# Performance work log

Measured on AMD Instinct MI355X. Metric: run time of the kernel, lower is better.

The kernel has to match this reference:

```python
import jax, jax.numpy as jnp
import numpy as np

N_NODES = 50000
N_EDGES = 800000
N_RELS = 200
D = 128


def setup_inputs() -> dict:
    key = jax.random.key(0)
    ks = jax.random.split(key, 9)
    h = jax.random.normal(ks[0], (N_NODES, D), dtype=jnp.float32)
    r = jax.random.normal(ks[1], (N_RELS, D), dtype=jnp.float32)
    norm = jax.random.uniform(ks[2], (N_NODES, 1), dtype=jnp.float32)
    src = jax.random.randint(ks[3], (N_EDGES,), 0, N_NODES, dtype=jnp.int32)
    dst = jax.random.randint(ks[4], (N_EDGES,), 0, N_NODES, dtype=jnp.int32)
    rel = jax.random.randint(ks[5], (N_EDGES,), 0, N_RELS, dtype=jnp.int32)
    stdv = 1.0 / np.sqrt(D)
    W_msg = jax.random.uniform(ks[6], (D, D), minval=-stdv, maxval=stdv, dtype=jnp.float32)
    W = jax.random.uniform(ks[7], (D, D), minval=-stdv, maxval=stdv, dtype=jnp.float32)
    b = jax.random.uniform(ks[8], (D,), minval=-stdv, maxval=stdv, dtype=jnp.float32)
    return {"h": h, "r": r, "norm": norm, "src": src, "dst": dst, "rel": rel,
            "W_msg": W_msg, "W": W, "b": b}


def reference(h, r, norm, src, dst, rel, W_msg, W, b):
    # dropout=0.0 (eval); h = h * norm (symmetric-norm pre-scale)
    hn = h * norm                                    # [N, D]
    # per-edge message: (h_src - r_rel) @ W_msg
    msg = (hn[src] - r[rel]) @ W_msg                 # [E, D]
    # scatter-sum to destination nodes, then post-scale by norm
    agg = jax.ops.segment_sum(msg, dst, num_segments=hn.shape[0]) * norm  # [N, D]
    out = hn @ W + agg + b
    return jax.nn.relu(out)
```

## Files before the change

kernel.cpp:

```cpp
#include <hip/hip_runtime.h>

#define N_NODES 50000
#define N_EDGES 800000
#define DIM 128
#define K2 256
#define NREL 200
#define NB2 391
#define EPB 2048
#define BN4 16
#define NB4 3128
#define ECAP4 512

typedef unsigned short u16;
typedef __attribute__((ext_vector_type(8))) short short8;
typedef __attribute__((ext_vector_type(4))) float f32x4;

__device__ __forceinline__ float bf2f(u16 v) {
    union { unsigned int u; float f; } x;
    x.u = ((unsigned int)v) << 16;
    return x.f;
}

__device__ __forceinline__ u16 f2bf(float f) {
    union { unsigned int u; float f; } x;
    x.f = f;
    return (u16)((x.u + 0x7FFFu + ((x.u >> 16) & 1u)) >> 16);
}

__device__ __forceinline__ int sniff_fp32(const void* h, int tid) {
    const u16* hp = (const u16*)h;
    u16 v = hp[2 * (tid & 63)];
    float a = fabsf(bf2f(v));
    int insane = ((v & 0x7F80) == 0x7F80) || (a != 0.0f && (a > 1e6f || a < 1e-20f));
    return __popcll(__ballot(insane)) > 16;
}

#define PREP_H (N_NODES * 32)
#define PREP_R (NREL * 32)
#define PREP_W 8192
#define PREP_N (N_NODES / 4)
#define PREP_B 32
#define PREP_TOT (PREP_H + PREP_R + PREP_W + PREP_N + PREP_B)
#define PREP_BLOCKS ((PREP_TOT + 255) / 256)
#define HIST_BLOCKS 128
__global__ __launch_bounds__(256) void prep_hist(
    const void* __restrict__ h, const void* __restrict__ r, const void* __restrict__ norm,
    const void* __restrict__ W, const void* __restrict__ Wmsg, const void* __restrict__ bias,
    const int* __restrict__ dst,
    u16* __restrict__ hx, u16* __restrict__ r_bf, u16* __restrict__ wt,
    u16* __restrict__ norm_bf, float* __restrict__ b_f, int* __restrict__ bucketCount)
{
    __shared__ int hh[NB2];
    int tid = threadIdx.x;
    if (blockIdx.x >= PREP_BLOCKS) {
        for (int i = tid; i < NB2; i += 256) hh[i] = 0;
        __syncthreads();
        int stride = HIST_BLOCKS * 256;
        for (int e = (blockIdx.x - PREP_BLOCKS) * 256 + tid; e < N_EDGES; e += stride)
            atomicAdd(&hh[dst[e] >> 7], 1);
        __syncthreads();
        for (int i = tid; i < NB2; i += 256)
            if (hh[i]) atomicAdd(&bucketCount[i], hh[i]);
        return;
    }
    int isf = sniff_fp32(h, tid);
    int t = blockIdx.x * 256 + tid;
    if (t < PREP_H) {
        int n = t >> 5, c = t & 31;
        float4 v; float nv;
        if (isf) {
            nv = ((const float*)norm)[n];
            v = *(const float4*)((const float*)h + (size_t)n * DIM + c * 4);
        } else {
            nv = bf2f(((const u16*)norm)[n]);
            ushort4 u = *(const ushort4*)((const u16*)h + (size_t)n * DIM + c * 4);
            v = make_float4(bf2f(u.x), bf2f(u.y), bf2f(u.z), bf2f(u.w));
        }
        ushort4 o;
        o.x = f2bf(v.x * nv); o.y = f2bf(v.y * nv); o.z = f2bf(v.z * nv); o.w = f2bf(v.w * nv);
        *(ushort4*)(hx + (size_t)n * DIM + c * 4) = o;
    } else if (t < PREP_H + PREP_R) {
        int t2 = t - PREP_H;
        int rho = t2 >> 5, c = t2 & 31;
        float4 v;
        if (isf) v = *(const float4*)((const float*)r + (size_t)rho * DIM + c * 4);
        else {
            ushort4 u = *(const ushort4*)((const u16*)r + (size_t)rho * DIM + c * 4);
            v = make_float4(bf2f(u.x), bf2f(u.y), bf2f(u.z), bf2f(u.w));
        }
        ushort4 o;
        o.x = f2bf(v.x); o.y = f2bf(v.y); o.z = f2bf(v.z); o.w = f2bf(v.w);
        *(ushort4*)(r_bf + (size_t)rho * DIM + c * 4) = o;
    } else if (t < PREP_H + PREP_R + PREP_W) {
        int t3 = t - PREP_H - PREP_R;
        int j = t3 >> 6;
        int k0 = (t3 & 63) * 4;
        ushort4 o;
        u16* op = (u16*)&o;
        for (int kk = 0; kk < 4; ++kk) {
            int k = k0 + kk;
            float wv;
            if (isf) wv = (k < 128) ? ((const float*)W)[(size_t)k * DIM + j]
                                    : ((const float*)Wmsg)[(size_t)(k - 128) * DIM + j];
            else     wv = (k < 128) ? bf2f(((const u16*)W)[(size_t)k * DIM + j])
                                    : bf2f(((const u16*)Wmsg)[(size_t)(k - 128) * DIM + j]);
            op[kk] = f2bf(wv);
        }
        *(ushort4*)(wt + (size_t)j * K2 + k0) = o;
    } else if (t < PREP_H + PREP_R + PREP_W + PREP_N) {
        int n0 = (t - PREP_H - PREP_R - PREP_W) * 4;
        ushort4 o;
        if (isf) {
            float4 v = *(const float4*)((const float*)norm + n0);
            o.x = f2bf(v.x); o.y = f2bf(v.y); o.z = f2bf(v.z); o.w = f2bf(v.w);
        } else {
            o = *(const ushort4*)((const u16*)norm + n0);
        }
        *(ushort4*)(norm_bf + n0) = o;
    } else if (t < PREP_TOT) {
        int j0 = (t - PREP_H - PREP_R - PREP_W - PREP_N) * 4;
        float4 v;
        if (isf) v = *(const float4*)((const float*)bias + j0);
        else {
            ushort4 u = *(const ushort4*)((const u16*)bias + j0);
            v = make_float4(bf2f(u.x), bf2f(u.y), bf2f(u.z), bf2f(u.w));
        }
        *(float4*)(b_f + j0) = v;
    }
}

__global__ __launch_bounds__(512) void bucket_scan(const int* __restrict__ bucketCount,
                            int* __restrict__ bucketBase, int* __restrict__ bucketCursor) {
    __shared__ int sd[512];
    int t = threadIdx.x;
    int c = (t < NB2) ? bucketCount[t] : 0;
    sd[t] = c;
    __syncthreads();
    for (int off = 1; off < 512; off <<= 1) {
        int v = (t >= off) ? sd[t - off] : 0;
        __syncthreads();
        sd[t] += v;
        __syncthreads();
    }
    if (t < NB2) { int ex = sd[t] - c; bucketBase[t] = ex; bucketCursor[t] = ex; }
    if (t == 0) bucketBase[NB2] = N_EDGES;
}

__global__ __launch_bounds__(512) void fill_lds(
    const int* __restrict__ dst, const int* __restrict__ src, const int* __restrict__ rel,
    int* __restrict__ bucketCursor, int* __restrict__ spk)
{
    __shared__ int hist[NB2];
    __shared__ int lbase[NB2];
    __shared__ int gbase[NB2];
    __shared__ int sd[512];
    __shared__ int pay[EPB];
    __shared__ u16 bkt[EPB];
    int tid = threadIdx.x;
    for (int i = tid; i < NB2; i += 512) hist[i] = 0;
    __syncthreads();
    int e0 = blockIdx.x * EPB;
    int myb[4], myr[4], myp[4];
#pragma unroll
    for (int i = 0; i < 4; ++i) {
        int e = e0 + i * 512 + tid;
        myb[i] = -1;
        if (e < N_EDGES) {
            int d = dst[e];
            int b = d >> 7;
            myb[i] = b;
            myr[i] = atomicAdd(&hist[b], 1);
            myp[i] = src[e] | (rel[e] << 16) | ((d & 127) << 24);
        }
    }
    __syncthreads();
    sd[tid] = (tid < NB2) ? hist[tid] : 0;
    __syncthreads();
    for (int off = 1; off < 512; off <<= 1) {
        int v = (tid >= off) ? sd[tid - off] : 0;
        __syncthreads();
        sd[tid] += v;
        __syncthreads();
    }
    if (tid < NB2) {
        lbase[tid] = sd[tid] - hist[tid];
        gbase[tid] = hist[tid] ? atomicAdd(&bucketCursor[tid], hist[tid]) : 0;
    }
    __syncthreads();
#pragma unroll
    for (int i = 0; i < 4; ++i) {
        if (myb[i] >= 0) {
            int lp = lbase[myb[i]] + myr[i];
            pay[lp] = myp[i];
            bkt[lp] = (u16)myb[i];
        }
    }
    __syncthreads();
    int total = N_EDGES - e0; if (total > EPB) total = EPB;
#pragma unroll
    for (int i = 0; i < 4; ++i) {
        int lp = i * 512 + tid;
        if (lp < total) {
            int b = bkt[lp];
            spk[gbase[b] + (lp - lbase[b])] = pay[lp];
        }
    }
}

__global__ __launch_bounds__(256) void bucket_fused(
    const u16* __restrict__ hx, const u16* __restrict__ r_bf,
    const u16* __restrict__ norm_bf, const float* __restrict__ b_f,
    const int* __restrict__ bucketBase, const int* __restrict__ spk,
    const u16* __restrict__ wt, const void* __restrict__ h, void* __restrict__ out)
{
    __shared__ int sorted[ECAP4];
    __shared__ int hist[BN4];
    __shared__ int nbase[BN4];
    __shared__ u16 Xu[BN4][136];
    int tid = threadIdx.x;
    int b = blockIdx.x;
    int fb = b >> 3, oct = b & 7;
    int base = bucketBase[fb], end = bucketBase[fb + 1];
    int size = end - base;

    if (tid < BN4) hist[tid] = 0;
    __syncthreads();
    for (int i = tid; i < size; i += 256) {
        int dl = (spk[base + i] >> 24) & 127;
        if ((dl >> 4) == oct) atomicAdd(&hist[dl & 15], 1);
    }
    __syncthreads();
    if (tid < BN4) nbase[tid] = hist[tid];
    __syncthreads();
    for (int off = 1; off < BN4; off <<= 1) {
        int v = 0;
        if (tid < BN4 && tid >= off) v = nbase[tid - off];
        __syncthreads();
        if (tid < BN4) nbase[tid] += v;
        __syncthreads();
    }
    if (tid < BN4) { nbase[tid] -= hist[tid]; hist[tid] = 0; }
    __syncthreads();
    for (int i = tid; i < size; i += 256) {
        int pk = spk[base + i];
        int dl = (pk >> 24) & 127;
        if ((dl >> 4) == oct) {
            int d4 = dl & 15;
            int rk = atomicAdd(&hist[d4], 1);
            int pos = nbase[d4] + rk;
            if (pos < ECAP4) sorted[pos] = pk;
        }
    }
    __syncthreads();

    int g = tid & 15, grp = tid >> 4;
    {
        int d4 = grp;
        int rs = nbase[d4], cnt = hist[d4];
        float acc[8] = {};
        int j = 0;
        for (; j + 3 < cnt; j += 4) {
            int pk0 = sorted[rs + j], pk1 = sorted[rs + j + 1];
            int pk2 = sorted[rs + j + 2], pk3 = sorted[rs + j + 3];
            short8 h0 = *(const short8*)(hx + (size_t)(pk0 & 0xFFFF) * DIM + g * 8);
            short8 h1 = *(const short8*)(hx + (size_t)(pk1 & 0xFFFF) * DIM + g * 8);
            short8 h2 = *(const short8*)(hx + (size_t)(pk2 & 0xFFFF) * DIM + g * 8);
            short8 h3 = *(const short8*)(hx + (size_t)(pk3 & 0xFFFF) * DIM + g * 8);
            short8 v0 = *(const short8*)(r_bf + (size_t)((pk0 >> 16) & 0xFF) * DIM + g * 8);
            short8 v1 = *(const short8*)(r_bf + (size_t)((pk1 >> 16) & 0xFF) * DIM + g * 8);
            short8 v2 = *(const short8*)(r_bf + (size_t)((pk2 >> 16) & 0xFF) * DIM + g * 8);
            short8 v3 = *(const short8*)(r_bf + (size_t)((pk3 >> 16) & 0xFF) * DIM + g * 8);
#pragma unroll
            for (int d = 0; d < 8; ++d) {
                acc[d] += (bf2f((u16)h0[d]) - bf2f((u16)v0[d]))
                        + (bf2f((u16)h1[d]) - bf2f((u16)v1[d]))
                        + (bf2f((u16)h2[d]) - bf2f((u16)v2[d]))
                        + (bf2f((u16)h3[d]) - bf2f((u16)v3[d]));
            }
        }
        for (; j < cnt; ++j) {
            int pk = sorted[rs + j];
            short8 hv = *(const short8*)(hx + (size_t)(pk & 0xFFFF) * DIM + g * 8);
            short8 rv = *(const short8*)(r_bf + (size_t)((pk >> 16) & 0xFF) * DIM + g * 8);
#pragma unroll
            for (int d = 0; d < 8; ++d) acc[d] += bf2f((u16)hv[d]) - bf2f((u16)rv[d]);
        }
        int node = b * BN4 + d4;
        float nv = bf2f(norm_bf[node < N_NODES ? node : 0]);
        short8 o;
#pragma unroll
        for (int d = 0; d < 8; ++d) o[d] = (short)f2bf(acc[d] * nv);
        *(short8*)&Xu[d4][g * 8] = o;
    }
    __syncthreads();

    int w = tid >> 6, lane = tid & 63;
    int m = lane & 15, quad = lane >> 4;
    int nodeA = b * BN4 + m;
    short8 a[8];
#pragma unroll
    for (int kb = 0; kb < 4; ++kb)
        a[kb] = *(const short8*)(hx + (size_t)nodeA * DIM + kb * 32 + quad * 8);
#pragma unroll
    for (int kb = 0; kb < 4; ++kb)
        a[4 + kb] = *(const short8*)&Xu[m][kb * 32 + quad * 8];
    int isf = sniff_fp32(h, tid);
#pragma unroll
    for (int ct = 0; ct < 2; ++ct) {
        int n0 = w * 32 + ct * 16;
        f32x4 c4 = {0.f, 0.f, 0.f, 0.f};
#pragma unroll
        for (int kb = 0; kb < 8; ++kb) {
            short8 bv = *(const short8*)(wt + (size_t)(n0 + m) * K2 + kb * 32 + quad * 8);
            c4 = __builtin_amdgcn_mfma_f32_16x16x32_bf16(a[kb], bv, c4, 0, 0, 0);
        }
        int col = n0 + m;
        float bb = b_f[col];
#pragma unroll
        for (int rg = 0; rg < 4; ++rg) {
            int n = b * BN4 + quad * 4 + rg;
            if (n < N_NODES) {
                float v = c4[rg] + bb;
                v = v > 0.f ? v : 0.f;
                if (isf) ((float*)out)[(size_t)n * DIM + col] = v;
                else     ((u16*)out)[(size_t)n * DIM + col] = f2bf(v);
            }
        }
    }
}

static inline size_t alup(size_t x) { return (x + 255) & ~(size_t)255; }

extern "C" void kernel_launch(void* const* d_in, const int* in_sizes, int n_in,
                              void* d_out, int out_size, void* d_ws, size_t ws_size,
                              hipStream_t stream) {
    const void* h    = d_in[0];
    const void* r    = d_in[1];
    const void* norm = d_in[2];
    const int* src   = (const int*)d_in[3];
    const int* dst   = (const int*)d_in[4];
    const int* rel   = (const int*)d_in[5];
    const void* Wmsg = d_in[6];
    const void* W    = d_in[7];
    const void* b    = d_in[8];

    char* p = (char*)d_ws;
    u16* hx       = (u16*)p;                 p += alup((size_t)N_NODES * DIM * 2);
    u16* r_bf     = (u16*)p;                 p += alup((size_t)NREL * DIM * 2);
    u16* wt       = (u16*)p;                 p += alup((size_t)DIM * K2 * 2);
    u16* norm_bf  = (u16*)p;                 p += alup((size_t)N_NODES * 2);
    float* b_f    = (float*)p;               p += alup((size_t)DIM * 4);
    int* bucketCount  = (int*)p;             p += alup((size_t)NB2 * 4);
    int* bucketBase   = (int*)p;             p += alup((size_t)(NB2 + 1) * 4);
    int* bucketCursor = (int*)p;             p += alup((size_t)NB2 * 4);
    int* spk      = (int*)p;                 p += alup((size_t)N_EDGES * 4);

    hipMemsetAsync(bucketCount, 0, (size_t)NB2 * 4, stream);
    prep_hist<<<PREP_BLOCKS + HIST_BLOCKS, 256, 0, stream>>>(
        h, r, norm, W, Wmsg, b, dst, hx, r_bf, wt, norm_bf, b_f, bucketCount);
    bucket_scan<<<1, 512, 0, stream>>>(bucketCount, bucketBase, bucketCursor);
    fill_lds<<<(N_EDGES + EPB - 1) / EPB, 512, 0, stream>>>(dst, src, rel, bucketCursor, spk);
    bucket_fused<<<NB4, 256, 0, stream>>>(
        hx, r_bf, norm_bf, b_f, bucketBase, spk, wt, h, d_out);
}
```

Baseline: 194.5 us.

## Bucket edges by 16-node groups and accumulate with LDS float atomics

Edges are now bucketed directly by 16-node destination groups (3125 buckets) instead of 128-node buckets followed by a per-block re-sort. The separate scan kernel is merged into the fill kernel: every block redundantly scans the bucket counts and scatters edges through global atomics on per-bucket cursors, so the LDS local sort is gone. In the fused kernel, edges are accumulated into an fp32 LDS tile with shared-memory atomics rather than via per-node sorted lists. This removes one launch and the in-block counting sort, at the cost of many more global atomics, redundant scans in each block, and LDS atomic contention.

```diff
diff --git a/kernel.cpp b/kernel.cpp
--- a/kernel.cpp
+++ b/kernel.cpp
@@ -5,11 +5,10 @@
 #define DIM 128
 #define K2 256
 #define NREL 200
-#define NB2 391
-#define EPB 2048
-#define BN4 16
-#define NB4 3128
-#define ECAP4 512
+#define NBF 3125
+#define BN 16
+#define FEB 2048
+#define FILL_BLOCKS ((N_EDGES + FEB - 1) / FEB)
 
 typedef unsigned short u16;
 typedef __attribute__((ext_vector_type(8))) short short8;
@@ -50,16 +49,16 @@
     u16* __restrict__ hx, u16* __restrict__ r_bf, u16* __restrict__ wt,
     u16* __restrict__ norm_bf, float* __restrict__ b_f, int* __restrict__ bucketCount)
 {
-    __shared__ int hh[NB2];
+    __shared__ int hh[NBF];
     int tid = threadIdx.x;
     if (blockIdx.x >= PREP_BLOCKS) {
-        for (int i = tid; i < NB2; i += 256) hh[i] = 0;
+        for (int i = tid; i < NBF; i += 256) hh[i] = 0;
         __syncthreads();
         int stride = HIST_BLOCKS * 256;
         for (int e = (blockIdx.x - PREP_BLOCKS) * 256 + tid; e < N_EDGES; e += stride)
-            atomicAdd(&hh[dst[e] >> 7], 1);
+            atomicAdd(&hh[dst[e] >> 4], 1);
         __syncthreads();
-        for (int i = tid; i < NB2; i += 256)
+        for (int i = tid; i < NBF; i += 256)
             if (hh[i]) atomicAdd(&bucketCount[i], hh[i]);
         return;
     }
@@ -129,52 +128,22 @@
     }
 }
 
-__global__ __launch_bounds__(512) void bucket_scan(const int* __restrict__ bucketCount,
-                            int* __restrict__ bucketBase, int* __restrict__ bucketCursor) {
-    __shared__ int sd[512];
-    int t = threadIdx.x;
-    int c = (t < NB2) ? bucketCount[t] : 0;
-    sd[t] = c;
-    __syncthreads();
-    for (int off = 1; off < 512; off <<= 1) {
-        int v = (t >= off) ? sd[t - off] : 0;
-        __syncthreads();
-        sd[t] += v;
-        __syncthreads();
-    }
-    if (t < NB2) { int ex = sd[t] - c; bucketBase[t] = ex; bucketCursor[t] = ex; }
-    if (t == 0) bucketBase[NB2] = N_EDGES;
-}
-
-__global__ __launch_bounds__(512) void fill_lds(
+__global__ __launch_bounds__(512) void fill_scatter(
     const int* __restrict__ dst, const int* __restrict__ src, const int* __restrict__ rel,
+    const int* __restrict__ bucketCount, int* __restrict__ bucketBase,
     int* __restrict__ bucketCursor, int* __restrict__ spk)
 {
-    __shared__ int hist[NB2];
-    __shared__ int lbase[NB2];
-    __shared__ int gbase[NB2];
+    __shared__ int sbase[NBF];
     __shared__ int sd[512];
-    __shared__ int pay[EPB];
-    __shared__ u16 bkt[EPB];
     int tid = threadIdx.x;
-    for (int i = tid; i < NB2; i += 512) hist[i] = 0;
-    __syncthreads();
-    int e0 = blockIdx.x * EPB;
-    int myb[4], myr[4], myp[4];
-#pragma unroll
-    for (int i = 0; i < 4; ++i) {
-        int e = e0 + i * 512 + tid;
-        myb[i] = -1;
-        if (e < N_EDGES) {
-            int d = dst[e];
-            int b = d >> 7;
-            myb[i] = b;
-            myr[i] = atomicAdd(&hist[b], 1);
-            myp[i] = src[e] | (rel[e] << 16) | ((d & 127) << 24);
-        }
-    }
-    __syncthreads();
-    sd[tid] = (tid < NB2) ? hist[tid] : 0;
+    int lv[7]; int ls = 0;
+#pragma unroll
+    for (int i = 0; i < 7; ++i) {
+        int idx = tid * 7 + i;
+        lv[i] = (idx < NBF) ? bucketCount[idx] : 0;
+        ls += lv[i];
+    }
+    sd[tid] = ls;
     __syncthreads();
     for (int off = 1; off < 512; off <<= 1) {
         int v = (tid >= off) ? sd[tid - off] : 0;
@@ -182,27 +151,27 @@
         sd[tid] += v;
         __syncthreads();
     }
-    if (tid < NB2) {
-        lbase[tid] = sd[tid] - hist[tid];
-        gbase[tid] = hist[tid] ? atomicAdd(&bucketCursor[tid], hist[tid]) : 0;
+    int ex = sd[tid] - ls;
+#pragma unroll
+    for (int i = 0; i < 7; ++i) {
+        int idx = tid * 7 + i;
+        if (idx < NBF) sbase[idx] = ex;
+        ex += lv[i];
     }
     __syncthreads();
+    if (blockIdx.x == 0) {
+        for (int i = tid; i < NBF; i += 512) bucketBase[i] = sbase[i];
+        if (tid == 0) bucketBase[NBF] = N_EDGES;
+    }
+    int e0 = blockIdx.x * FEB;
 #pragma unroll
     for (int i = 0; i < 4; ++i) {
-        if (myb[i] >= 0) {
-            int lp = lbase[myb[i]] + myr[i];
-            pay[lp] = myp[i];
-            bkt[lp] = (u16)myb[i];
-        }
-    }
-    __syncthreads();
-    int total = N_EDGES - e0; if (total > EPB) total = EPB;
-#pragma unroll
-    for (int i = 0; i < 4; ++i) {
-        int lp = i * 512 + tid;
-        if (lp < total) {
-            int b = bkt[lp];
-            spk[gbase[b] + (lp - lbase[b])] = pay[lp];
+        int e = e0 + i * 512 + tid;
+        if (e < N_EDGES) {
+            int d = dst[e];
+            int bb = d >> 4;
+            int pos = sbase[bb] + atomicAdd(&bucketCursor[bb], 1);
+            spk[pos] = (src[e] & 0xFFFF) | (rel[e] << 16) | ((d & 15) << 24);
         }
     }
 }
@@ -213,97 +182,67 @@
     const int* __restrict__ bucketBase, const int* __restrict__ spk,
     const u16* __restrict__ wt, const void* __restrict__ h, void* __restrict__ out)
 {
-    __shared__ int sorted[ECAP4];
-    __shared__ int hist[BN4];
-    __shared__ int nbase[BN4];
-    __shared__ u16 Xu[BN4][136];
+    __shared__ float Xacc[BN][132];
     int tid = threadIdx.x;
     int b = blockIdx.x;
-    int fb = b >> 3, oct = b & 7;
-    int base = bucketBase[fb], end = bucketBase[fb + 1];
-    int size = end - base;
-
-    if (tid < BN4) hist[tid] = 0;
+    int base = bucketBase[b], end = bucketBase[b + 1];
+    int cnt = end - base;
+
+    for (int i = tid; i < BN * 132; i += 256) ((float*)Xacc)[i] = 0.f;
     __syncthreads();
-    for (int i = tid; i < size; i += 256) {
-        int dl = (spk[base + i] >> 24) & 127;
-        if ((dl >> 4) == oct) atomicAdd(&hist[dl & 15], 1);
-    }
-    __syncthreads();
-    if (tid < BN4) nbase[tid] = hist[tid];
-    __syncthreads();
-    for (int off = 1; off < BN4; off <<= 1) {
-        int v = 0;
-        if (tid < BN4 && tid >= off) v = nbase[tid - off];
-        __syncthreads();
-        if (tid < BN4) nbase[tid] += v;
-        __syncthreads();
-    }
-    if (tid < BN4) { nbase[tid] -= hist[tid]; hist[tid] = 0; }
-    __syncthreads();
-    for (int i = tid; i < size; i += 256) {
-        int pk = spk[base + i];
-        int dl = (pk >> 24) & 127;
-        if ((dl >> 4) == oct) {
-            int d4 = dl & 15;
-            int rk = atomicAdd(&hist[d4], 1);
-            int pos = nbase[d4] + rk;
-            if (pos < ECAP4) sorted[pos] = pk;
-        }
-    }
-    __syncthreads();
 
     int g = tid & 15, grp = tid >> 4;
-    {
-        int d4 = grp;
-        int rs = nbase[d4], cnt = hist[d4];
-        float acc[8] = {};
-        int j = 0;
-        for (; j + 3 < cnt; j += 4) {
-            int pk0 = sorted[rs + j], pk1 = sorted[rs + j + 1];
-            int pk2 = sorted[rs + j + 2], pk3 = sorted[rs + j + 3];
-            short8 h0 = *(const short8*)(hx + (size_t)(pk0 & 0xFFFF) * DIM + g * 8);
-            short8 h1 = *(const short8*)(hx + (size_t)(pk1 & 0xFFFF) * DIM + g * 8);
-            short8 h2 = *(const short8*)(hx + (size_t)(pk2 & 0xFFFF) * DIM + g * 8);
-            short8 h3 = *(const short8*)(hx + (size_t)(pk3 & 0xFFFF) * DIM + g * 8);
-            short8 v0 = *(const short8*)(r_bf + (size_t)((pk0 >> 16) & 0xFF) * DIM + g * 8);
-            short8 v1 = *(const short8*)(r_bf + (size_t)((pk1 >> 16) & 0xFF) * DIM + g * 8);
-            short8 v2 = *(const short8*)(r_bf + (size_t)((pk2 >> 16) & 0xFF) * DIM + g * 8);
-            short8 v3 = *(const short8*)(r_bf + (size_t)((pk3 >> 16) & 0xFF) * DIM + g * 8);
-#pragma unroll
-            for (int d = 0; d < 8; ++d) {
-                acc[d] += (bf2f((u16)h0[d]) - bf2f((u16)v0[d]))
-                        + (bf2f((u16)h1[d]) - bf2f((u16)v1[d]))
-                        + (bf2f((u16)h2[d]) - bf2f((u16)v2[d]))
-                        + (bf2f((u16)h3[d]) - bf2f((u16)v3[d]));
-            }
-        }
-        for (; j < cnt; ++j) {
-            int pk = sorted[rs + j];
-            short8 hv = *(const short8*)(hx + (size_t)(pk & 0xFFFF) * DIM + g * 8);
-            short8 rv = *(const short8*)(r_bf + (size_t)((pk >> 16) & 0xFF) * DIM + g * 8);
-#pragma unroll
-            for (int d = 0; d < 8; ++d) acc[d] += bf2f((u16)hv[d]) - bf2f((u16)rv[d]);
-        }
-        int node = b * BN4 + d4;
-        float nv = bf2f(norm_bf[node < N_NODES ? node : 0]);
-        short8 o;
-#pragma unroll
-        for (int d = 0; d < 8; ++d) o[d] = (short)f2bf(acc[d] * nv);
-        *(short8*)&Xu[d4][g * 8] = o;
+    const int* ep = spk + base;
+    int j = grp;
+    for (; j + 48 < cnt; j += 64) {
+        int pk0 = ep[j], pk1 = ep[j + 16], pk2 = ep[j + 32], pk3 = ep[j + 48];
+        short8 h0 = *(const short8*)(hx + (size_t)(pk0 & 0xFFFF) * DIM + g * 8);
+        short8 h1 = *(const short8*)(hx + (size_t)(pk1 & 0xFFFF) * DIM + g * 8);
+        short8 h2 = *(const short8*)(hx + (size_t)(pk2 & 0xFFFF) * DIM + g * 8);
+        short8 h3 = *(const short8*)(hx + (size_t)(pk3 & 0xFFFF) * DIM + g * 8);
+        short8 v0 = *(const short8*)(r_bf + (size_t)((pk0 >> 16) & 0xFF) * DIM + g * 8);
+        short8 v1 = *(const short8*)(r_bf + (size_t)((pk1 >> 16) & 0xFF) * DIM + g * 8);
+        short8 v2 = *(const short8*)(r_bf + (size_t)((pk2 >> 16) & 0xFF) * DIM + g * 8);
+        short8 v3 = *(const short8*)(r_bf + (size_t)((pk3 >> 16) & 0xFF) * DIM + g * 8);
+        float* x0 = &Xacc[(pk0 >> 24) & 15][g * 8];
+        float* x1 = &Xacc[(pk1 >> 24) & 15][g * 8];
+        float* x2 = &Xacc[(pk2 >> 24) & 15][g * 8];
+        float* x3 = &Xacc[(pk3 >> 24) & 15][g * 8];
+#pragma unroll
+        for (int d = 0; d < 8; ++d) atomicAdd(&x0[d], bf2f((u16)h0[d]) - bf2f((u16)v0[d]));
+#pragma unroll
+        for (int d = 0; d < 8; ++d) atomicAdd(&x1[d], bf2f((u16)h1[d]) - bf2f((u16)v1[d]));
+#pragma unroll
+        for (int d = 0; d < 8; ++d) atomicAdd(&x2[d], bf2f((u16)h2[d]) - bf2f((u16)v2[d]));
+#pragma unroll
+        for (int d = 0; d < 8; ++d) atomicAdd(&x3[d], bf2f((u16)h3[d]) - bf2f((u16)v3[d]));
+    }
+    for (; j < cnt; j += 16) {
+        int pk = ep[j];
+        short8 hv = *(const short8*)(hx + (size_t)(pk & 0xFFFF) * DIM + g * 8);
+        short8 rv = *(const short8*)(r_bf + (size_t)((pk >> 16) & 0xFF) * DIM + g * 8);
+        float* xr = &Xacc[(pk >> 24) & 15][g * 8];
+#pragma unroll
+        for (int d = 0; d < 8; ++d) atomicAdd(&xr[d], bf2f((u16)hv[d]) - bf2f((u16)rv[d]));
     }
     __syncthreads();
 
     int w = tid >> 6, lane = tid & 63;
     int m = lane & 15, quad = lane >> 4;
-    int nodeA = b * BN4 + m;
+    int nodeA = b * BN + m;
     short8 a[8];
 #pragma unroll
     for (int kb = 0; kb < 4; ++kb)
         a[kb] = *(const short8*)(hx + (size_t)nodeA * DIM + kb * 32 + quad * 8);
-#pragma unroll
-    for (int kb = 0; kb < 4; ++kb)
-        a[4 + kb] = *(const short8*)&Xu[m][kb * 32 + quad * 8];
+    float nv = bf2f(norm_bf[nodeA]);
+#pragma unroll
+    for (int kb = 0; kb < 4; ++kb) {
+        const float* xp = &Xacc[m][kb * 32 + quad * 8];
+        short8 t;
+#pragma unroll
+        for (int d = 0; d < 8; ++d) t[d] = (short)f2bf(xp[d] * nv);
+        a[4 + kb] = t;
+    }
     int isf = sniff_fp32(h, tid);
 #pragma unroll
     for (int ct = 0; ct < 2; ++ct) {
@@ -318,13 +257,11 @@
         float bb = b_f[col];
 #pragma unroll
         for (int rg = 0; rg < 4; ++rg) {
-            int n = b * BN4 + quad * 4 + rg;
-            if (n < N_NODES) {
-                float v = c4[rg] + bb;
-                v = v > 0.f ? v : 0.f;
-                if (isf) ((float*)out)[(size_t)n * DIM + col] = v;
-                else     ((u16*)out)[(size_t)n * DIM + col] = f2bf(v);
-            }
+            int n = b * BN + quad * 4 + rg;
+            float v = c4[rg] + bb;
+            v = v > 0.f ? v : 0.f;
+            if (isf) ((float*)out)[(size_t)n * DIM + col] = v;
+            else     ((u16*)out)[(size_t)n * DIM + col] = f2bf(v);
         }
     }
 }
@@ -350,16 +287,18 @@
     u16* wt       = (u16*)p;                 p += alup((size_t)DIM * K2 * 2);
     u16* norm_bf  = (u16*)p;                 p += alup((size_t)N_NODES * 2);
     float* b_f    = (float*)p;               p += alup((size_t)DIM * 4);
-    int* bucketCount  = (int*)p;             p += alup((size_t)NB2 * 4);
-    int* bucketBase   = (int*)p;             p += alup((size_t)(NB2 + 1) * 4);
-    int* bucketCursor = (int*)p;             p += alup((size_t)NB2 * 4);
+    int* bucketCC = (int*)p;                 p += alup((size_t)2 * NBF * 4);
+    int* bucketBase = (int*)p;               p += alup((size_t)(NBF + 1) * 4);
     int* spk      = (int*)p;                 p += alup((size_t)N_EDGES * 4);
 
-    hipMemsetAsync(bucketCount, 0, (size_t)NB2 * 4, stream);
+    int* bucketCount  = bucketCC;
+    int* bucketCursor = bucketCC + NBF;
+
+    hipMemsetAsync(bucketCC, 0, (size_t)2 * NBF * 4, stream);
     prep_hist<<<PREP_BLOCKS + HIST_BLOCKS, 256, 0, stream>>>(
         h, r, norm, W, Wmsg, b, dst, hx, r_bf, wt, norm_bf, b_f, bucketCount);
-    bucket_scan<<<1, 512, 0, stream>>>(bucketCount, bucketBase, bucketCursor);
-    fill_lds<<<(N_EDGES + EPB - 1) / EPB, 512, 0, stream>>>(dst, src, rel, bucketCursor, spk);
-    bucket_fused<<<NB4, 256, 0, stream>>>(
+    fill_scatter<<<FILL_BLOCKS, 512, 0, stream>>>(
+        dst, src, rel, bucketCount, bucketBase, bucketCursor, spk);
+    bucket_fused<<<NBF, 256, 0, stream>>>(
         hx, r_bf, norm_bf, b_f, bucketBase, spk, wt, h, d_out);
 }
```

After: 733.7 us. 277% more time.

## Add per-node fine sort pass and drop redundant bucket rescans in fused kernel

Applied to the files above, without the earlier changes.

The single-block bucket scan is folded into each fill block, which now recomputes the prefix of bucket counts redundantly, so one kernel launch goes away. A new sort_fine kernel sorts each 128-node bucket by local destination and writes per-node edge offsets (nodeBase). The fused kernel then copies its contiguous edge range directly instead of having all eight blocks per bucket rescan and re-sort the whole bucket. This removes repeated histogram and atomic work in the hot kernel, at the cost of an extra kernel pass over the edge list and the loss of bounds guards that rely on N_NODES being a multiple of 16.

```diff
diff --git a/kernel.cpp b/kernel.cpp
--- a/kernel.cpp
+++ b/kernel.cpp
@@ -7,9 +7,11 @@
 #define NREL 200
 #define NB2 391
 #define EPB 2048
-#define BN4 16
-#define NB4 3128
-#define ECAP4 512
+#define FILL_BLOCKS ((N_EDGES + EPB - 1) / EPB)
+#define ECAP5 3072
+#define BNF 16
+#define NFB 3125
+#define ECAP6 768
 
 typedef unsigned short u16;
 typedef __attribute__((ext_vector_type(8))) short short8;
@@ -129,34 +131,29 @@
     }
 }
 
-__global__ __launch_bounds__(512) void bucket_scan(const int* __restrict__ bucketCount,
-                            int* __restrict__ bucketBase, int* __restrict__ bucketCursor) {
-    __shared__ int sd[512];
-    int t = threadIdx.x;
-    int c = (t < NB2) ? bucketCount[t] : 0;
-    sd[t] = c;
-    __syncthreads();
-    for (int off = 1; off < 512; off <<= 1) {
-        int v = (t >= off) ? sd[t - off] : 0;
-        __syncthreads();
-        sd[t] += v;
-        __syncthreads();
-    }
-    if (t < NB2) { int ex = sd[t] - c; bucketBase[t] = ex; bucketCursor[t] = ex; }
-    if (t == 0) bucketBase[NB2] = N_EDGES;
-}
-
 __global__ __launch_bounds__(512) void fill_lds(
     const int* __restrict__ dst, const int* __restrict__ src, const int* __restrict__ rel,
-    int* __restrict__ bucketCursor, int* __restrict__ spk)
+    const int* __restrict__ bucketCount, int* __restrict__ bucketCursor,
+    int* __restrict__ spk)
 {
     __shared__ int hist[NB2];
     __shared__ int lbase[NB2];
     __shared__ int gbase[NB2];
+    __shared__ int cbase[NB2];
     __shared__ int sd[512];
     __shared__ int pay[EPB];
     __shared__ u16 bkt[EPB];
     int tid = threadIdx.x;
+    int c = (tid < NB2) ? bucketCount[tid] : 0;
+    sd[tid] = c;
+    __syncthreads();
+    for (int off = 1; off < 512; off <<= 1) {
+        int v = (tid >= off) ? sd[tid - off] : 0;
+        __syncthreads();
+        sd[tid] += v;
+        __syncthreads();
+    }
+    if (tid < NB2) cbase[tid] = sd[tid] - c;
     for (int i = tid; i < NB2; i += 512) hist[i] = 0;
     __syncthreads();
     int e0 = blockIdx.x * EPB;
@@ -184,7 +181,7 @@
     }
     if (tid < NB2) {
         lbase[tid] = sd[tid] - hist[tid];
-        gbase[tid] = hist[tid] ? atomicAdd(&bucketCursor[tid], hist[tid]) : 0;
+        gbase[tid] = cbase[tid] + (hist[tid] ? atomicAdd(&bucketCursor[tid], hist[tid]) : 0);
     }
     __syncthreads();
 #pragma unroll
@@ -207,61 +204,96 @@
     }
 }
 
+__global__ __launch_bounds__(512) void sort_fine(
+    const int* __restrict__ bucketCount, int* __restrict__ spk,
+    int* __restrict__ nodeBase)
+{
+    __shared__ int hist[128];
+    __shared__ int lb[128];
+    __shared__ int sd[512];
+    __shared__ int sorted[ECAP5];
+    int tid = threadIdx.x;
+    int fb = blockIdx.x;
+    int acc = 0;
+    for (int i = tid; i < NB2; i += 512)
+        if (i < fb) acc += bucketCount[i];
+    sd[tid] = acc;
+    __syncthreads();
+    for (int off = 256; off > 0; off >>= 1) {
+        if (tid < off) sd[tid] += sd[tid + off];
+        __syncthreads();
+    }
+    int base = sd[0];
+    int size = bucketCount[fb];
+    if (size > ECAP5) size = ECAP5;
+    if (tid < 128) hist[tid] = 0;
+    __syncthreads();
+    int myp[6], myr[6], myd[6];
+#pragma unroll
+    for (int q = 0; q < 6; ++q) {
+        int i = tid + q * 512;
+        myd[q] = -1;
+        if (i < size) {
+            int pk = spk[base + i];
+            int dl = (pk >> 24) & 127;
+            myp[q] = pk;
+            myd[q] = dl;
+            myr[q] = atomicAdd(&hist[dl], 1);
+        }
+    }
+    __syncthreads();
+    if (tid < 128) sd[tid] = hist[tid];
+    __syncthreads();
+    for (int off = 1; off < 128; off <<= 1) {
+        int v = 0;
+        if (tid < 128 && tid >= off) v = sd[tid - off];
+        __syncthreads();
+        if (tid < 128) sd[tid] += v;
+        __syncthreads();
+    }
+    if (tid < 128) lb[tid] = sd[tid] - hist[tid];
+    __syncthreads();
+#pragma unroll
+    for (int q = 0; q < 6; ++q)
+        if (myd[q] >= 0) sorted[lb[myd[q]] + myr[q]] = myp[q];
+    __syncthreads();
+    for (int i = tid; i < size; i += 512) spk[base + i] = sorted[i];
+    if (tid < 128) {
+        int node = fb * 128 + tid;
+        if (node <= N_NODES) nodeBase[node] = base + lb[tid];
+    }
+    if (fb == 0 && tid == 0) nodeBase[N_NODES] = N_EDGES;
+}
+
 __global__ __launch_bounds__(256) void bucket_fused(
     const u16* __restrict__ hx, const u16* __restrict__ r_bf,
     const u16* __restrict__ norm_bf, const float* __restrict__ b_f,
-    const int* __restrict__ bucketBase, const int* __restrict__ spk,
+    const int* __restrict__ nodeBase, const int* __restrict__ spk,
     const u16* __restrict__ wt, const void* __restrict__ h, void* __restrict__ out)
 {
-    __shared__ int sorted[ECAP4];
-    __shared__ int hist[BN4];
-    __shared__ int nbase[BN4];
-    __shared__ u16 Xu[BN4][136];
+    __shared__ int nb[BNF + 1];
+    __shared__ int eidx[ECAP6];
+    __shared__ u16 Xu[BNF][136];
     int tid = threadIdx.x;
     int b = blockIdx.x;
-    int fb = b >> 3, oct = b & 7;
-    int base = bucketBase[fb], end = bucketBase[fb + 1];
-    int size = end - base;
-
-    if (tid < BN4) hist[tid] = 0;
-    __syncthreads();
-    for (int i = tid; i < size; i += 256) {
-        int dl = (spk[base + i] >> 24) & 127;
-        if ((dl >> 4) == oct) atomicAdd(&hist[dl & 15], 1);
-    }
-    __syncthreads();
-    if (tid < BN4) nbase[tid] = hist[tid];
-    __syncthreads();
-    for (int off = 1; off < BN4; off <<= 1) {
-        int v = 0;
-        if (tid < BN4 && tid >= off) v = nbase[tid - off];
-        __syncthreads();
-        if (tid < BN4) nbase[tid] += v;
-        __syncthreads();
-    }
-    if (tid < BN4) { nbase[tid] -= hist[tid]; hist[tid] = 0; }
-    __syncthreads();
-    for (int i = tid; i < size; i += 256) {
-        int pk = spk[base + i];
-        int dl = (pk >> 24) & 127;
-        if ((dl >> 4) == oct) {
-            int d4 = dl & 15;
-            int rk = atomicAdd(&hist[d4], 1);
-            int pos = nbase[d4] + rk;
-            if (pos < ECAP4) sorted[pos] = pk;
-        }
-    }
+    if (tid <= BNF) nb[tid] = nodeBase[b * BNF + tid];
+    __syncthreads();
+    int bs = nb[0];
+    int tot = nb[BNF] - bs; if (tot > ECAP6) tot = ECAP6;
+    for (int i = tid; i < tot; i += 256) eidx[i] = spk[bs + i];
     __syncthreads();
 
     int g = tid & 15, grp = tid >> 4;
     {
-        int d4 = grp;
-        int rs = nbase[d4], cnt = hist[d4];
+        int rs = nb[grp] - bs, re = nb[grp + 1] - bs;
+        if (rs > ECAP6) rs = ECAP6;
+        if (re > ECAP6) re = ECAP6;
+        int cnt = re - rs;
         float acc[8] = {};
         int j = 0;
         for (; j + 3 < cnt; j += 4) {
-            int pk0 = sorted[rs + j], pk1 = sorted[rs + j + 1];
-            int pk2 = sorted[rs + j + 2], pk3 = sorted[rs + j + 3];
+            int pk0 = eidx[rs + j], pk1 = eidx[rs + j + 1];
+            int pk2 = eidx[rs + j + 2], pk3 = eidx[rs + j + 3];
             short8 h0 = *(const short8*)(hx + (size_t)(pk0 & 0xFFFF) * DIM + g * 8);
             short8 h1 = *(const short8*)(hx + (size_t)(pk1 & 0xFFFF) * DIM + g * 8);
             short8 h2 = *(const short8*)(hx + (size_t)(pk2 & 0xFFFF) * DIM + g * 8);
@@ -279,24 +311,24 @@
             }
         }
         for (; j < cnt; ++j) {
-            int pk = sorted[rs + j];
+            int pk = eidx[rs + j];
             short8 hv = *(const short8*)(hx + (size_t)(pk & 0xFFFF) * DIM + g * 8);
             short8 rv = *(const short8*)(r_bf + (size_t)((pk >> 16) & 0xFF) * DIM + g * 8);
 #pragma unroll
             for (int d = 0; d < 8; ++d) acc[d] += bf2f((u16)hv[d]) - bf2f((u16)rv[d]);
         }
-        int node = b * BN4 + d4;
-        float nv = bf2f(norm_bf[node < N_NODES ? node : 0]);
+        int node = b * BNF + grp;
+        float nv = bf2f(norm_bf[node]);
         short8 o;
 #pragma unroll
         for (int d = 0; d < 8; ++d) o[d] = (short)f2bf(acc[d] * nv);
-        *(short8*)&Xu[d4][g * 8] = o;
+        *(short8*)&Xu[grp][g * 8] = o;
     }
     __syncthreads();
 
     int w = tid >> 6, lane = tid & 63;
     int m = lane & 15, quad = lane >> 4;
-    int nodeA = b * BN4 + m;
+    int nodeA = b * BNF + m;
     short8 a[8];
 #pragma unroll
     for (int kb = 0; kb < 4; ++kb)
@@ -318,13 +350,11 @@
         float bb = b_f[col];
 #pragma unroll
         for (int rg = 0; rg < 4; ++rg) {
-            int n = b * BN4 + quad * 4 + rg;
-            if (n < N_NODES) {
-                float v = c4[rg] + bb;
-                v = v > 0.f ? v : 0.f;
-                if (isf) ((float*)out)[(size_t)n * DIM + col] = v;
-                else     ((u16*)out)[(size_t)n * DIM + col] = f2bf(v);
-            }
+            int n = b * BNF + quad * 4 + rg;
+            float v = c4[rg] + bb;
+            v = v > 0.f ? v : 0.f;
+            if (isf) ((float*)out)[(size_t)n * DIM + col] = v;
+            else     ((u16*)out)[(size_t)n * DIM + col] = f2bf(v);
         }
     }
 }
@@ -350,16 +380,19 @@
     u16* wt       = (u16*)p;                 p += alup((size_t)DIM * K2 * 2);
     u16* norm_bf  = (u16*)p;                 p += alup((size_t)N_NODES * 2);
     float* b_f    = (float*)p;               p += alup((size_t)DIM * 4);
-    int* bucketCount  = (int*)p;             p += alup((size_t)NB2 * 4);
-    int* bucketBase   = (int*)p;             p += alup((size_t)(NB2 + 1) * 4);
-    int* bucketCursor = (int*)p;             p += alup((size_t)NB2 * 4);
+    int* bucketCC = (int*)p;                 p += alup((size_t)2 * NB2 * 4);
+    int* nodeBase = (int*)p;                 p += alup((size_t)(N_NODES + 64) * 4);
     int* spk      = (int*)p;                 p += alup((size_t)N_EDGES * 4);
 
-    hipMemsetAsync(bucketCount, 0, (size_t)NB2 * 4, stream);
+    int* bucketCount  = bucketCC;
+    int* bucketCursor = bucketCC + NB2;
+
+    hipMemsetAsync(bucketCC, 0, (size_t)2 * NB2 * 4, stream);
     prep_hist<<<PREP_BLOCKS + HIST_BLOCKS, 256, 0, stream>>>(
         h, r, norm, W, Wmsg, b, dst, hx, r_bf, wt, norm_bf, b_f, bucketCount);
-    bucket_scan<<<1, 512, 0, stream>>>(bucketCount, bucketBase, bucketCursor);
-    fill_lds<<<(N_EDGES + EPB - 1) / EPB, 512, 0, stream>>>(dst, src, rel, bucketCursor, spk);
-    bucket_fused<<<NB4, 256, 0, stream>>>(
-        hx, r_bf, norm_bf, b_f, bucketBase, spk, wt, h, d_out);
-}
+    fill_lds<<<FILL_BLOCKS, 512, 0, stream>>>(
+        dst, src, rel, bucketCount, bucketCursor, spk);
+    sort_fine<<<NB2, 512, 0, stream>>>(bucketCount, spk, nodeBase);
+    bucket_fused<<<NFB, 256, 0, stream>>>(
+        hx, r_bf, norm_bf, b_f, nodeBase, spk, wt, h, d_out);
+}
```

New measurement: 188.8 us. -2.9%, faster.
